# Kernel tuning notes

Measured on AMD Instinct MI355X. Metric: run time of the kernel, lower is better.

The kernel has to match this reference:

```python
import jax, jax.numpy as jnp
import numpy as np

NUM_LEVELS = 16
MIN_RES = 16
MAX_RES = 4096
LOG2_HASHMAP_SIZE = 19
FEATURES_PER_LEVEL = 2
TABLE_SIZE = 1 << LOG2_HASHMAP_SIZE
HASH_INIT_SCALE = 0.001
N_POINTS = 1 << 20

_growth = np.exp((np.log(MAX_RES) - np.log(MIN_RES)) / (NUM_LEVELS - 1))
SCALINGS = jnp.asarray(np.floor(MIN_RES * _growth ** np.arange(NUM_LEVELS)), dtype=jnp.float32)  # [L]
HASH_OFFSET = jnp.arange(NUM_LEVELS, dtype=jnp.int32) * TABLE_SIZE  # [L]
PRIMES = jnp.array([1, 2654435761, 805459861], dtype=jnp.uint32)
# corner selection (1 -> ceil, 0 -> floor) matching hashed_0..hashed_7 in the torch code
CORNER_MASK = jnp.array([[1,1,1],[1,0,1],[0,0,1],[0,1,1],[1,1,0],[1,0,0],[0,0,0],[0,1,0]], dtype=bool)


def _hash(coords):
    # coords: int32 [..., L, 3]. torch uses int64 products, but since TABLE_SIZE
    # is a power of two dividing 2^32, uint32 wraparound is bit-identical mod TABLE_SIZE.
    u = coords.astype(jnp.uint32) * PRIMES
    h = u[..., 0] ^ u[..., 1] ^ u[..., 2]
    h = h & jnp.uint32(TABLE_SIZE - 1)
    return h.astype(jnp.int32) + HASH_OFFSET  # [..., L]


def setup_inputs() -> dict:
    key = jax.random.key(0)
    kx, kt = jax.random.split(key)
    x = jax.random.uniform(kx, (N_POINTS, 3), dtype=jnp.float32)
    hash_table = (jax.random.uniform(kt, (TABLE_SIZE * NUM_LEVELS, FEATURES_PER_LEVEL),
                                     dtype=jnp.float32) * 2.0 - 1.0) * HASH_INIT_SCALE
    return {"x": x, "hash_table": hash_table}


def reference(x, hash_table):
    # x: [N, 3] in [0,1]; hash_table: [TABLE_SIZE*L, F]
    scaled = x[:, None, :] * SCALINGS[None, :, None]          # [N, L, 3]
    scaled_f = jnp.floor(scaled)
    scaled_c = jnp.ceil(scaled)
    offset = scaled - scaled_f                                 # [N, L, 3]
    cf = scaled_f.astype(jnp.int32)
    cc = scaled_c.astype(jnp.int32)
    corners = jnp.where(CORNER_MASK[:, None, None, :], cc[None], cf[None])  # [8, N, L, 3]
    idx = _hash(corners)                                       # [8, N, L]
    f = hash_table[idx]                                        # [8, N, L, F]
    ox, oy, oz = offset[..., 0:1], offset[..., 1:2], offset[..., 2:3]
    f03 = f[0] * ox + f[3] * (1 - ox)
    f12 = f[1] * ox + f[2] * (1 - ox)
    f56 = f[5] * ox + f[6] * (1 - ox)
    f47 = f[4] * ox + f[7] * (1 - ox)
    f0312 = f03 * oy + f12 * (1 - oy)
    f4756 = f47 * oy + f56 * (1 - oy)
    enc = f0312 * oz + f4756 * (1 - oz)                        # [N, L, F]
    return enc.reshape(enc.shape[0], NUM_LEVELS * FEATURES_PER_LEVEL)  # [N, L*F]
```

## Files before the change

### kernel.cpp

```cpp
#include <hip/hip_runtime.h>
#include <hip/hip_fp16.h>
#include <math.h>

#define NPTS   (1u << 20)
#define NLVL   16
#define NGRID  5
#define TBITS  19
#define TSIZE  (1u << TBITS)
#define TMASK  (TSIZE - 1u)
#define CHUNKS (NPTS / 256u)
#define PR1    2654435761u
#define PR2    805459861u

typedef float vf4 __attribute__((ext_vector_type(4)));

struct Params {
    float    s[NLVL];
    uint32_t gdim[NGRID];
    uint32_t goff[NGRID];
    uint32_t vcum[NGRID + 1];
};

__device__ __forceinline__ float2 h2f_bits(float bits)
{
    __half2 h; __builtin_memcpy(&h, &bits, 4);
    return __half22float2(h);
}

__device__ __forceinline__ void issue_pair_h(const __half2* __restrict__ t,
                                             uint32_t iF, uint32_t iC,
                                             float2& q, float& a, float& b,
                                             bool& merged, bool& swp)
{
    const uint32_t lo = iF < iC ? iF : iC;
    const uint32_t hi = iF < iC ? iC : iF;
    merged = (hi - lo == 1u);
    swp    = merged && (iF == hi);
    if (merged) {
        asm volatile("global_load_dwordx2 %0, %1, off sc0"
                     : "=v"(q) : "v"(t + lo));
    } else {
        asm volatile("global_load_dword %0, %1, off sc0"
                     : "=v"(a) : "v"(t + iF));
        asm volatile("global_load_dword %0, %1, off sc0"
                     : "=v"(b) : "v"(t + iC));
    }
}

__device__ __forceinline__ float2 sel_Fh(const float2& q, float a, bool m, bool s)
{ return m ? h2f_bits(s ? q.y : q.x) : h2f_bits(a); }
__device__ __forceinline__ float2 sel_Ch(const float2& q, float b, bool m, bool s)
{ return m ? h2f_bits(s ? q.x : q.y) : h2f_bits(b); }

__device__ __forceinline__ float2 lerp8(float2 f0, float2 f1, float2 f2, float2 f3,
                                        float2 f4, float2 f5, float2 f6, float2 f7,
                                        float ox, float oy, float oz)
{
    const float omx = 1.0f - ox, omy = 1.0f - oy, omz = 1.0f - oz;
    const float a0 = f0.x * ox + f3.x * omx, b0 = f0.y * ox + f3.y * omx;
    const float a1 = f1.x * ox + f2.x * omx, b1 = f1.y * ox + f2.y * omx;
    const float a2 = f5.x * ox + f6.x * omx, b2 = f5.y * ox + f6.y * omx;
    const float a3 = f4.x * ox + f7.x * omx, b3 = f4.y * ox + f7.y * omx;
    const float c0 = a0 * oy + a1 * omy, d0 = b0 * oy + b1 * omy;
    const float c1 = a3 * oy + a2 * omy, d1 = b3 * oy + b2 * omy;
    return make_float2(c0 * oz + c1 * omz, d0 * oz + d1 * omz);
}

__device__ __forceinline__ float2 eval_hash_h(float x0, float x1, float x2,
                                              float s, uint32_t l,
                                              const __half2* __restrict__ th)
{
    const float sx = x0 * s, sy = x1 * s, sz = x2 * s;
    const float fxf = floorf(sx), fyf = floorf(sy), fzf = floorf(sz);
    const float cxf = ceilf(sx),  cyf = ceilf(sy),  czf = ceilf(sz);
    const float ox = sx - fxf, oy = sy - fyf, oz = sz - fzf;

    const uint32_t fx = (uint32_t)fxf, cx = (uint32_t)cxf;
    const uint32_t Yf = (uint32_t)fyf * PR1,  Yc = (uint32_t)cyf * PR1;
    const uint32_t Zf = (uint32_t)fzf * PR2,  Zc = (uint32_t)czf * PR2;
    const uint32_t base = l << TBITS;

    const uint32_t i0 = ((cx ^ Yc ^ Zc) & TMASK) + base;
    const uint32_t i1 = ((cx ^ Yf ^ Zc) & TMASK) + base;
    const uint32_t i2 = ((fx ^ Yf ^ Zc) & TMASK) + base;
    const uint32_t i3 = ((fx ^ Yc ^ Zc) & TMASK) + base;
    const uint32_t i4 = ((cx ^ Yc ^ Zf) & TMASK) + base;
    const uint32_t i5 = ((cx ^ Yf ^ Zf) & TMASK) + base;
    const uint32_t i6 = ((fx ^ Yf ^ Zf) & TMASK) + base;
    const uint32_t i7 = ((fx ^ Yc ^ Zf) & TMASK) + base;

    float2 qA, qB, qC, qD;
    float aA, bA, aB, bB, aC, bC, aD, bD;
    bool mA, sA, mB, sB, mC, sC, mD, sD;
    issue_pair_h(th, i3, i0, qA, aA, bA, mA, sA);
    issue_pair_h(th, i2, i1, qB, aB, bB, mB, sB);
    issue_pair_h(th, i7, i4, qC, aC, bC, mC, sC);
    issue_pair_h(th, i6, i5, qD, aD, bD, mD, sD);
    asm volatile("s_waitcnt vmcnt(0)" ::: "memory");
    __builtin_amdgcn_sched_barrier(0);

    const float2 f3 = sel_Fh(qA, aA, mA, sA), f0 = sel_Ch(qA, bA, mA, sA);
    const float2 f2 = sel_Fh(qB, aB, mB, sB), f1 = sel_Ch(qB, bB, mB, sB);
    const float2 f7 = sel_Fh(qC, aC, mC, sC), f4 = sel_Ch(qC, bC, mC, sC);
    const float2 f6 = sel_Fh(qD, aD, mD, sD), f5 = sel_Ch(qD, bD, mD, sD);
    return lerp8(f0, f1, f2, f3, f4, f5, f6, f7, ox, oy, oz);
}

__device__ __forceinline__ float2 eval_grid_h(float x0, float x1, float x2,
                                              float s,
                                              const __half2* __restrict__ g,
                                              uint32_t d)
{
    const float sx = x0 * s, sy = x1 * s, sz = x2 * s;
    const float fxf = floorf(sx), fyf = floorf(sy), fzf = floorf(sz);
    const float cxf = ceilf(sx),  cyf = ceilf(sy),  czf = ceilf(sz);
    const float ox = sx - fxf, oy = sy - fyf, oz = sz - fzf;

    const uint32_t fx = (uint32_t)fxf, fy = (uint32_t)fyf, fz = (uint32_t)fzf;
    const uint32_t cy = (uint32_t)cyf, cz = (uint32_t)czf;
    const bool xadj = ((uint32_t)cxf == fx + 1u);

    const uint32_t bA = (cz * d + cy) * d + fx;
    const uint32_t bB = (cz * d + fy) * d + fx;
    const uint32_t bC = (fz * d + cy) * d + fx;
    const uint32_t bD = (fz * d + fy) * d + fx;

    float2 qA, qB, qC, qD;
    asm volatile("global_load_dwordx2 %0, %1, off sc0" : "=v"(qA) : "v"(g + bA));
    asm volatile("global_load_dwordx2 %0, %1, off sc0" : "=v"(qB) : "v"(g + bB));
    asm volatile("global_load_dwordx2 %0, %1, off sc0" : "=v"(qC) : "v"(g + bC));
    asm volatile("global_load_dwordx2 %0, %1, off sc0" : "=v"(qD) : "v"(g + bD));
    asm volatile("s_waitcnt vmcnt(0)" ::: "memory");
    __builtin_amdgcn_sched_barrier(0);

    const float2 f3 = h2f_bits(qA.x);
    const float2 f0 = xadj ? h2f_bits(qA.y) : f3;
    const float2 f2 = h2f_bits(qB.x);
    const float2 f1 = xadj ? h2f_bits(qB.y) : f2;
    const float2 f7 = h2f_bits(qC.x);
    const float2 f4 = xadj ? h2f_bits(qC.y) : f7;
    const float2 f6 = h2f_bits(qD.x);
    const float2 f5 = xadj ? h2f_bits(qD.y) : f6;
    return lerp8(f0, f1, f2, f3, f4, f5, f6, f7, ox, oy, oz);
}

__global__ __launch_bounds__(256)
void convert_table(const float2* __restrict__ t, __half2* __restrict__ th)
{
    const uint32_t i = (blockIdx.x * 256u + threadIdx.x) * 4u;
    const float4 q0 = *(const float4*)(t + i);
    const float4 q1 = *(const float4*)(t + i + 2);
    __half2 h0 = __floats2half2_rn(q0.x, q0.y);
    __half2 h1 = __floats2half2_rn(q0.z, q0.w);
    __half2 h2 = __floats2half2_rn(q1.x, q1.y);
    __half2 h3 = __floats2half2_rn(q1.z, q1.w);
    uint32_t u0, u1, u2, u3;
    __builtin_memcpy(&u0, &h0, 4); __builtin_memcpy(&u1, &h1, 4);
    __builtin_memcpy(&u2, &h2, 4); __builtin_memcpy(&u3, &h3, 4);
    uint4 v; v.x = u0; v.y = u1; v.z = u2; v.w = u3;
    *(uint4*)(th + i) = v;
}

__global__ __launch_bounds__(256)
void build_grids(const float2* __restrict__ table, __half2* __restrict__ gridbuf,
                 Params P)
{
    const uint32_t t = blockIdx.x * 256u + threadIdx.x;
    if (t >= P.vcum[NGRID]) return;
    uint32_t l = 0;
    #pragma unroll
    for (int i = 1; i < NGRID; ++i) if (t >= P.vcum[i]) l = i;
    const uint32_t v = t - P.vcum[l];
    const uint32_t d = P.gdim[l];
    const uint32_t vz = v / (d * d);
    const uint32_t r1 = v - vz * d * d;
    const uint32_t vy = r1 / d;
    const uint32_t vx = r1 - vy * d;
    const uint32_t h = ((vx ^ (vy * PR1) ^ (vz * PR2)) & TMASK) + (l << TBITS);
    const float2 e = table[h];
    gridbuf[P.goff[l] + v] = __floats2half2_rn(e.x, e.y);
}

__global__ __launch_bounds__(256)
void gather16(const float* __restrict__ x,
              const __half2* __restrict__ th,
              const __half2* __restrict__ gridbuf,
              __half2* __restrict__ stage,
              Params P)
{
    const uint32_t l = blockIdx.x / CHUNKS;
    const uint32_t p = (blockIdx.x % CHUNKS) * 256u + threadIdx.x;

    const float x0 = x[p * 3 + 0];
    const float x1 = x[p * 3 + 1];
    const float x2 = x[p * 3 + 2];

    float2 e;
    if (l < NGRID)
        e = eval_grid_h(x0, x1, x2, P.s[l], gridbuf + P.goff[l], P.gdim[l]);
    else
        e = eval_hash_h(x0, x1, x2, P.s[l], l, th);

    stage[l * NPTS + p] = __floats2half2_rn(e.x, e.y);
}

__global__ __launch_bounds__(256)
void transpose_kernel(const __half2* __restrict__ stage, float* __restrict__ out)
{
    const uint32_t e = blockIdx.x * 256u + threadIdx.x;
    const uint32_t p = e >> 3;
    const uint32_t j = e & 7u;
    const float2 a = __half22float2(stage[(2u*j)     * NPTS + p]);
    const float2 b = __half22float2(stage[(2u*j + 1) * NPTS + p]);
    vf4 v; v.x = a.x; v.y = a.y; v.z = b.x; v.w = b.y;
    __builtin_nontemporal_store(v, (vf4*)(out + (size_t)e * 4u));
}

__device__ __forceinline__ void load_pair_plain(const float2* __restrict__ t,
                                                uint32_t iF, uint32_t iC,
                                                float2& vF, float2& vC)
{
    const uint32_t lo = iF < iC ? iF : iC;
    const uint32_t hi = iF < iC ? iC : iF;
    if (hi - lo == 1u) {
        const float4 q = *(const float4*)(t + lo);
        if (iF == lo) { vF = make_float2(q.x, q.y); vC = make_float2(q.z, q.w); }
        else          { vF = make_float2(q.z, q.w); vC = make_float2(q.x, q.y); }
    } else {
        vF = t[iF]; vC = t[iC];
    }
}

__global__ __launch_bounds__(256)
void hashenc_fused(const float* __restrict__ x,
                   const float2* __restrict__ table,
                   float2* __restrict__ out,
                   Params P)
{
    const uint32_t tid = blockIdx.x * 256u + threadIdx.x;
    const uint32_t p = tid >> 4;
    const uint32_t l = tid & 15u;

    const float x0 = x[p*3+0], x1 = x[p*3+1], x2 = x[p*3+2];
    const float s  = P.s[l];
    const float sx = x0 * s, sy = x1 * s, sz = x2 * s;
    const float fxf = floorf(sx), fyf = floorf(sy), fzf = floorf(sz);
    const float cxf = ceilf(sx),  cyf = ceilf(sy),  czf = ceilf(sz);
    const float ox = sx - fxf, oy = sy - fyf, oz = sz - fzf;

    const uint32_t fx = (uint32_t)fxf, cx = (uint32_t)cxf;
    const uint32_t Yf = (uint32_t)fyf * PR1,  Yc = (uint32_t)cyf * PR1;
    const uint32_t Zf = (uint32_t)fzf * PR2,  Zc = (uint32_t)czf * PR2;
    const uint32_t base = l << TBITS;

    const uint32_t i0 = ((cx ^ Yc ^ Zc) & TMASK) + base;
    const uint32_t i1 = ((cx ^ Yf ^ Zc) & TMASK) + base;
    const uint32_t i2 = ((fx ^ Yf ^ Zc) & TMASK) + base;
    const uint32_t i3 = ((fx ^ Yc ^ Zc) & TMASK) + base;
    const uint32_t i4 = ((cx ^ Yc ^ Zf) & TMASK) + base;
    const uint32_t i5 = ((cx ^ Yf ^ Zf) & TMASK) + base;
    const uint32_t i6 = ((fx ^ Yf ^ Zf) & TMASK) + base;
    const uint32_t i7 = ((fx ^ Yc ^ Zf) & TMASK) + base;

    float2 f0, f1, f2, f3, f4, f5, f6, f7;
    load_pair_plain(table, i3, i0, f3, f0);
    load_pair_plain(table, i2, i1, f2, f1);
    load_pair_plain(table, i7, i4, f7, f4);
    load_pair_plain(table, i6, i5, f6, f5);
    out[p * 16u + l] = lerp8(f0, f1, f2, f3, f4, f5, f6, f7, ox, oy, oz);
}

extern "C" void kernel_launch(void* const* d_in, const int* in_sizes, int n_in,
                              void* d_out, int out_size, void* d_ws, size_t ws_size,
                              hipStream_t stream) {
    const float*  x     = (const float*)d_in[0];
    const float2* table = (const float2*)d_in[1];

    Params P;
    const double growth = exp((log(4096.0) - log(16.0)) / 15.0);
    for (int l = 0; l < NLVL; ++l)
        P.s[l] = (float)floor(16.0 * pow(growth, (double)l));

    uint32_t vtot = 0;
    for (int l = 0; l < NGRID; ++l) {
        const uint32_t d = (uint32_t)P.s[l] + 1u;
        P.gdim[l] = d;
        P.vcum[l] = vtot;
        P.goff[l] = vtot;
        vtot += d * d * d;
    }
    P.vcum[NGRID] = vtot;

    const size_t grid_bytes  = (((size_t)vtot * sizeof(__half2)) + 255u) & ~(size_t)255u;
    const size_t tabh_bytes  = (size_t)TSIZE * NLVL * sizeof(__half2);
    const size_t stage_bytes = (size_t)NPTS * NLVL * sizeof(__half2);
    const size_t ws_needed   = grid_bytes + tabh_bytes + stage_bytes;

    if (ws_size >= ws_needed) {
        __half2* gridbuf = (__half2*)d_ws;
        __half2* th      = (__half2*)((char*)d_ws + grid_bytes);
        __half2* stage   = (__half2*)((char*)d_ws + grid_bytes + tabh_bytes);

        dim3 b256(256u);
        hipLaunchKernelGGL(convert_table, dim3(TSIZE * NLVL / 1024u), b256, 0, stream,
                           table, th);
        hipLaunchKernelGGL(build_grids, dim3((vtot + 255u) / 256u), b256, 0, stream,
                           table, gridbuf, P);
        hipLaunchKernelGGL(gather16, dim3(NLVL * CHUNKS), b256, 0, stream,
                           x, th, gridbuf, stage, P);
        hipLaunchKernelGGL(transpose_kernel, dim3(NPTS * 8u / 256u), b256, 0, stream,
                           stage, (float*)d_out);
    } else {
        float2* out = (float2*)d_out;
        hipLaunchKernelGGL(hashenc_fused, dim3(NPTS * NLVL / 256u), dim3(256u), 0, stream,
                           x, table, out, P);
    }
}
```

Measured before the change: 318.5 us.

## Serve three coarsest dense-grid levels from LDS-resident lookup tables

Adds a templated kernel that copies a small dense grid level (17^3, 24^3, 34^3 half2 entries) into shared memory and interpolates many points per block from it. Levels 0-2 now run in three separate launches, and the main gather kernel covers only the remaining levels. The goal is to swap global/L2 gathers for LDS reads on the coarsest levels. In exchange it adds kernel launches, repeats the LUT load per block, and the 34^3 table (about 157 KB) may limit occupancy or exceed the LDS budget.

```diff
diff --git a/kernel.cpp b/kernel.cpp
--- a/kernel.cpp
+++ b/kernel.cpp
@@ -4,11 +4,13 @@
 
 #define NPTS   (1u << 20)
 #define NLVL   16
+#define NLDS   3
 #define NGRID  5
 #define TBITS  19
 #define TSIZE  (1u << TBITS)
 #define TMASK  (TSIZE - 1u)
 #define CHUNKS (NPTS / 256u)
+#define NMAIN  (NLVL - NLDS)
 #define PR1    2654435761u
 #define PR2    805459861u
 
@@ -24,6 +26,11 @@
 __device__ __forceinline__ float2 h2f_bits(float bits)
 {
     __half2 h; __builtin_memcpy(&h, &bits, 4);
+    return __half22float2(h);
+}
+__device__ __forceinline__ float2 h2f_u32(uint32_t u)
+{
+    __half2 h; __builtin_memcpy(&h, &u, 4);
     return __half22float2(h);
 }
 
@@ -142,6 +149,55 @@
     const float2 f6 = h2f_bits(qD.x);
     const float2 f5 = xadj ? h2f_bits(qD.y) : f6;
     return lerp8(f0, f1, f2, f3, f4, f5, f6, f7, ox, oy, oz);
+}
+
+template<int D, int PB>
+__global__ __launch_bounds__(256)
+void lds_grid_kernel(const float* __restrict__ x,
+                     const __half2* __restrict__ gridsrc,
+                     __half2* __restrict__ stage,
+                     float s)
+{
+    __shared__ uint32_t lut[D * D * D];
+    const uint32_t nv = (uint32_t)(D * D * D);
+    const uint32_t* src = (const uint32_t*)gridsrc;
+    for (uint32_t i = threadIdx.x; i < nv; i += 256u) lut[i] = src[i];
+    __syncthreads();
+
+    const uint32_t p0 = blockIdx.x * (uint32_t)PB;
+    #pragma unroll
+    for (int k = 0; k < PB / 256; ++k) {
+        const uint32_t p = p0 + (uint32_t)k * 256u + threadIdx.x;
+        const float x0 = x[p * 3 + 0];
+        const float x1 = x[p * 3 + 1];
+        const float x2 = x[p * 3 + 2];
+
+        const float sx = x0 * s, sy = x1 * s, sz = x2 * s;
+        const float fxf = floorf(sx), fyf = floorf(sy), fzf = floorf(sz);
+        const float cxf = ceilf(sx),  cyf = ceilf(sy),  czf = ceilf(sz);
+        const float ox = sx - fxf, oy = sy - fyf, oz = sz - fzf;
+
+        const uint32_t fx = (uint32_t)fxf, fy = (uint32_t)fyf, fz = (uint32_t)fzf;
+        const uint32_t cy = (uint32_t)cyf, cz = (uint32_t)czf;
+        const uint32_t xo = ((uint32_t)cxf == fx + 1u) ? 1u : 0u;
+
+        const uint32_t bA = (cz * D + cy) * D + fx;
+        const uint32_t bB = (cz * D + fy) * D + fx;
+        const uint32_t bC = (fz * D + cy) * D + fx;
+        const uint32_t bD = (fz * D + fy) * D + fx;
+
+        const float2 f3 = h2f_u32(lut[bA]);
+        const float2 f0 = xo ? h2f_u32(lut[bA + 1]) : f3;
+        const float2 f2 = h2f_u32(lut[bB]);
+        const float2 f1 = xo ? h2f_u32(lut[bB + 1]) : f2;
+        const float2 f7 = h2f_u32(lut[bC]);
+        const float2 f4 = xo ? h2f_u32(lut[bC + 1]) : f7;
+        const float2 f6 = h2f_u32(lut[bD]);
+        const float2 f5 = xo ? h2f_u32(lut[bD + 1]) : f6;
+
+        const float2 e = lerp8(f0, f1, f2, f3, f4, f5, f6, f7, ox, oy, oz);
+        stage[p] = __floats2half2_rn(e.x, e.y);
+    }
 }
 
 __global__ __launch_bounds__(256)
@@ -188,7 +244,7 @@
               __half2* __restrict__ stage,
               Params P)
 {
-    const uint32_t l = blockIdx.x / CHUNKS;
+    const uint32_t l = NLDS + blockIdx.x / CHUNKS;
     const uint32_t p = (blockIdx.x % CHUNKS) * 256u + threadIdx.x;
 
     const float x0 = x[p * 3 + 0];
@@ -296,7 +352,7 @@
     const size_t stage_bytes = (size_t)NPTS * NLVL * sizeof(__half2);
     const size_t ws_needed   = grid_bytes + tabh_bytes + stage_bytes;
 
-    if (ws_size >= ws_needed) {
+    if (ws_size >= ws_needed && P.gdim[0] == 17u && P.gdim[1] == 24u && P.gdim[2] == 34u) {
         __half2* gridbuf = (__half2*)d_ws;
         __half2* th      = (__half2*)((char*)d_ws + grid_bytes);
         __half2* stage   = (__half2*)((char*)d_ws + grid_bytes + tabh_bytes);
@@ -306,7 +362,13 @@
                            table, th);
         hipLaunchKernelGGL(build_grids, dim3((vtot + 255u) / 256u), b256, 0, stream,
                            table, gridbuf, P);
-        hipLaunchKernelGGL(gather16, dim3(NLVL * CHUNKS), b256, 0, stream,
+        hipLaunchKernelGGL((lds_grid_kernel<17, 512>),  dim3(NPTS / 512u),  b256, 0, stream,
+                           x, gridbuf + P.goff[0], stage + 0u * NPTS, P.s[0]);
+        hipLaunchKernelGGL((lds_grid_kernel<24, 1024>), dim3(NPTS / 1024u), b256, 0, stream,
+                           x, gridbuf + P.goff[1], stage + 1u * NPTS, P.s[1]);
+        hipLaunchKernelGGL((lds_grid_kernel<34, 2048>), dim3(NPTS / 2048u), b256, 0, stream,
+                           x, gridbuf + P.goff[2], stage + 2u * NPTS, P.s[2]);
+        hipLaunchKernelGGL(gather16, dim3(NMAIN * CHUNKS), b256, 0, stream,
                            x, th, gridbuf, stage, P);
         hipLaunchKernelGGL(transpose_kernel, dim3(NPTS * 8u / 256u), b256, 0, stream,
                            stage, (float*)d_out);
```

Result: slower. 332.8 us (+4.5%).
